# Kernel tuning notes

Hardware: AMD Instinct MI355X
Metric: run time of the kernel (lower is better)

## Reference

```python
import jax, jax.numpy as jnp
import numpy as np

ALPHA = 0.2      # leaky_alpha
GRAPH_ITR = 2    # graph_itr
ENC_LEN = 250    # output_begin_idx = encoder_sequence.shape[1]


def _char_embedding(ids, emb, conv_w, conv_b):
    # ids: [B,N,Wl] int -> char-CNN: embed, conv1d over word dim, relu, max-pool
    x = emb[ids]                                      # [B,N,Wl,E]
    B, N, Wl, E = x.shape
    x = x.reshape(B * N, Wl, E).transpose(0, 2, 1)    # [B*N, E, Wl]
    y = jax.lax.conv_general_dilated(x, conv_w, (1,), [(2, 2)],
                                     dimension_numbers=('NCH', 'OIH', 'NCH'))
    y = jax.nn.relu(y + conv_b[None, :, None])        # [B*N, F, Wl]
    return y.max(axis=2).reshape(B, N, -1)            # [B,N,F]


def _dynamic_graph(x, W0a, W0b, b0, W1, b1, Wout, bout):
    # Pairwise MLP on concat(x_i, x_j); first layer computed as split matmuls
    # so the [B,N,N,2d] concat is never materialized.
    hi = jnp.einsum('bnd,de->bne', x, W0a)            # [B,N,d]
    hj = jnp.einsum('bnd,de->bne', x, W0b)            # [B,N,d]
    h = jax.nn.relu(hi[:, :, None, :] + hj[:, None, :, :] + b0)   # [B,N,N,d]
    h = jax.nn.relu(jnp.einsum('bnme,ef->bnmf', h, W1) + b1)      # [B,N,N,d]
    return jax.nn.sigmoid(jnp.einsum('bnme,e->bnm', h, Wout[:, 0]) + bout[0])


def _gat(x, adj, W, a1, a2):
    # Multi-head GAT: per-head projection, additive attention, adjacency-masked softmax.
    Wh = jnp.einsum('bnd,hdk->bhnk', x, W)            # [B,H,N,hid]
    f1 = jnp.einsum('bhnk,hk->bhn', Wh, a1)
    f2 = jnp.einsum('bhnk,hk->bhn', Wh, a2)
    e = jax.nn.leaky_relu(f1[:, :, :, None] + f2[:, :, None, :], ALPHA)  # [B,H,N,N]
    e = jnp.where(adj[:, None, :, :] > 0, e, -9e15)
    attn = jax.nn.softmax(e, axis=-1)
    h = jax.nn.elu(jnp.einsum('bhnm,bhmk->bhnk', attn, Wh))
    B, H, N, K = h.shape
    return h.transpose(0, 2, 1, 3).reshape(B, N, H * K)  # concat heads -> [B,N,d]


def setup_inputs() -> dict:
    key = jax.random.key(0)
    ks = jax.random.split(key, 20)
    B, Le, Ld, Wl = 2, 250, 150, 16
    Vin, E, F, K = 128, 64, 128, 5
    H, hid, Vout = 8, 32, 5000
    d = H * hid  # 256
    s = lambda k, sh: jax.random.normal(k, sh, dtype=jnp.float32) * 0.05
    return {
        'encoder_sequence': jax.random.randint(ks[0], (B, Le, Wl), 0, Vin),
        'initial_decoder_sequence': jax.random.randint(ks[1], (B, Ld, Wl), 0, Vin),
        'fixed_graph': jax.random.randint(ks[2], (B, Le + Ld, Le + Ld), 0, 2),
        'char_emb': s(ks[3], (Vin, E)),
        'conv_w': s(ks[4], (F, E, K)),
        'conv_b': jnp.zeros((F,), jnp.float32),
        'hst_W': s(ks[5], (F, d)),
        'hst_b': jnp.zeros((d,), jnp.float32),
        'dg_W0a': s(ks[6], (d, d)),
        'dg_W0b': s(ks[7], (d, d)),
        'dg_b0': jnp.zeros((d,), jnp.float32),
        'dg_W1': s(ks[8], (d, d)),
        'dg_b1': jnp.zeros((d,), jnp.float32),
        'dg_Wout': s(ks[9], (d, 1)),
        'dg_bout': jnp.zeros((1,), jnp.float32),
        'att_W': s(ks[10], (H, d, hid)),
        'att_a1': s(ks[11], (H, hid)),
        'att_a2': s(ks[12], (H, hid)),
        'out_W': s(ks[13], (d, Vout)),
        'out_b': jnp.zeros((Vout,), jnp.float32),
    }


def reference(encoder_sequence, initial_decoder_sequence, fixed_graph,
              char_emb, conv_w, conv_b, hst_W, hst_b,
              dg_W0a, dg_W0b, dg_b0, dg_W1, dg_b1, dg_Wout, dg_bout,
              att_W, att_a1, att_a2, out_W, out_b):
    ids = jnp.concatenate([encoder_sequence, initial_decoder_sequence], axis=1)  # [B,N,Wl]
    x = _char_embedding(ids, char_emb, conv_w, conv_b)    # [B,N,F]
    x = x @ hst_W + hst_b                                 # [B,N,d]
    fixed = fixed_graph.astype(jnp.float32)
    for _ in range(GRAPH_ITR):
        dyn = _dynamic_graph(x, dg_W0a, dg_W0b, dg_b0, dg_W1, dg_b1, dg_Wout, dg_bout)
        adj = jnp.clip(dyn + fixed, 0.0, 1.0)             # combine dynamic + fixed graph
        x = _gat(x, adj, att_W, att_a1, att_a2)
    return x[:, ENC_LEN:, :] @ out_W + out_b              # [B, dec_len, Vout]
```

## Files before the change

### kernel.cpp

```cpp
#include <hip/hip_runtime.h>
#include <hip/hip_bf16.h>
#include <math.h>


__device__ __forceinline__ float bf2f_raw(unsigned int u) {
    union { unsigned int i; float f; } cv; cv.i = u << 16; return cv.f;
}
__device__ __forceinline__ unsigned short f2bf(float f) {
    __hip_bfloat16 h = __float2bfloat16(f);
    return *reinterpret_cast<unsigned short*>(&h);
}

__global__ __launch_bounds__(256) void k_prep(const float* emb, const float* convw,
                                              float* T, const float* W,
                                              unsigned short* Wb) {
    int bid = blockIdx.x, t = threadIdx.x;
    if (bid < 128) {
        int v = bid;
        __shared__ float er[64];
        if (t < 64) er[t] = emb[v * 64 + t];
        __syncthreads();
        if (t < 128) {
            float acc[5] = {0.f, 0.f, 0.f, 0.f, 0.f};
            const float* w = convw + t * 320;
            for (int e = 0; e < 64; ++e) {
                float xe = er[e];
#pragma unroll
                for (int k = 0; k < 5; ++k) acc[k] += xe * w[e * 5 + k];
            }
#pragma unroll
            for (int k = 0; k < 5; ++k) T[(k * 128 + v) * 128 + t] = acc[k];
        }
    } else {
        int i0 = (bid - 128) * 512 + t * 2;
        if (i0 < 256 * 5000) {
            float2 w2 = *reinterpret_cast<const float2*>(W + i0);
            unsigned int u = ((unsigned int)f2bf(w2.y) << 16) | f2bf(w2.x);
            *reinterpret_cast<unsigned int*>(Wb + i0) = u;
        }
    }
}

__global__ __launch_bounds__(256) void k_convhst(const int* enc, const int* dec,
                                                 const float* convb, const float* T,
                                                 const float* hstW, const float* hstb,
                                                 float* x) {
    int w = blockIdx.x, t = threadIdx.x;
    int b = w / 400, n = w % 400;
    __shared__ int ids[16];
    __shared__ float xcl[128];
    if (t < 16) {
        ids[t] = (n < 250) ? enc[(b * 250 + n) * 16 + t]
                           : dec[(b * 150 + (n - 250)) * 16 + t];
    }
    __syncthreads();
    if (t < 128) {
        float best = -1e30f;
        for (int p = 0; p < 16; ++p) {
            float s = 0.f;
#pragma unroll
            for (int k = 0; k < 5; ++k) {
                int q = p + k - 2;
                if (q >= 0 && q < 16) s += T[(k * 128 + ids[q]) * 128 + t];
            }
            best = fmaxf(best, s);
        }
        xcl[t] = fmaxf(best + convb[t], 0.f);
    }
    __syncthreads();
    float acc = hstb[t];
    for (int c = 0; c < 128; ++c) acc += xcl[c] * hstW[c * 256 + t];
    x[w * 256 + t] = acc;
}

__global__ __launch_bounds__(256) void k_wh(const float* x, const float* attW,
                                            const float* a1g, const float* a2g,
                                            float* Wh, float* f1, float* f2) {
    int blk = blockIdx.x, t = threadIdx.x;
    int w0 = blk * 2;
    int h = t >> 5, k = t & 31;
    __shared__ float xr[2][256];
    for (int i = t; i < 512; i += 256) xr[i >> 8][i & 255] = x[w0 * 256 + i];
    __syncthreads();
    float acc0 = 0.f, acc1 = 0.f;
    const float* Wp = attW + h * 8192 + k;
#pragma unroll 8
    for (int d = 0; d < 256; ++d) {
        float wv = Wp[d * 32];
        acc0 += xr[0][d] * wv;
        acc1 += xr[1][d] * wv;
    }
    float a1v = a1g[t], a2v = a2g[t];
    int b = w0 / 400;
    int bh = b * 8 + h;
    float accs[2] = {acc0, acc1};
#pragma unroll
    for (int rw = 0; rw < 2; ++rw) {
        int n = (w0 + rw) % 400;
        Wh[(bh * 400 + n) * 32 + k] = accs[rw];
        float v1 = accs[rw] * a1v, v2 = accs[rw] * a2v;
#pragma unroll
        for (int mm = 16; mm >= 1; mm >>= 1) {
            v1 += __shfl_xor(v1, mm, 64);
            v2 += __shfl_xor(v2, mm, 64);
        }
        if (k == 0) { f1[bh * 400 + n] = v1; f2[bh * 400 + n] = v2; }
    }
}

#define WST 36
__global__ __launch_bounds__(256) void k_attn(const float* Wh, const float* f1g,
                                              const float* f2g, float* xout) {
    int tile = blockIdx.x, bh = blockIdx.y;
    int b = bh >> 3, h = bh & 7;
    int t = threadIdx.x;
    int n0 = tile * 16;
    __shared__ float Whl[400 * WST];
    __shared__ float f2l[400];
    __shared__ float4 plT[400];
    __shared__ float f1l[16];
    __shared__ float red[4][8][4][4];
    __shared__ float sred[2][4][4];
    __shared__ float wmax[4];

    const float4* Whg4 = (const float4*)(Wh + bh * 12800);
    for (int i = t; i < 3200; i += 256) {
        float4 v = Whg4[i];
        int m = i >> 3, k4 = i & 7;
        *(float4*)&Whl[m * WST + k4 * 4] = v;
    }
    float fm = -1e30f;
    for (int m = t; m < 400; m += 256) {
        float v = f2g[bh * 400 + m];
        f2l[m] = v;
        fm = fmaxf(fm, v);
    }
    if (t < 16) f1l[t] = f1g[bh * 400 + n0 + t];
#pragma unroll
    for (int mm = 32; mm >= 1; mm >>= 1) fm = fmaxf(fm, __shfl_xor(fm, mm, 64));
    if ((t & 63) == 0) wmax[t >> 6] = fm;
    __syncthreads();
    float fmax2 = fmaxf(fmaxf(wmax[0], wmax[1]), fmaxf(wmax[2], wmax[3]));

    int g = t & 7, kq = (t >> 3) & 7, wv = t >> 6;
    int gm = g + 8 * wv;
    for (int it = 0; it < 4; ++it) {
        float f1a = f1l[it * 4 + 0], f1b = f1l[it * 4 + 1];
        float f1c = f1l[it * 4 + 2], f1d = f1l[it * 4 + 3];
        float rm0 = f1a + fmax2; rm0 = rm0 > 0.f ? rm0 : 0.2f * rm0;
        float rm1 = f1b + fmax2; rm1 = rm1 > 0.f ? rm1 : 0.2f * rm1;
        float rm2 = f1c + fmax2; rm2 = rm2 > 0.f ? rm2 : 0.2f * rm2;
        float rm3 = f1d + fmax2; rm3 = rm3 > 0.f ? rm3 : 0.2f * rm3;
        float ps0 = 0.f, ps1 = 0.f, ps2 = 0.f, ps3 = 0.f;
        for (int m = t; m < 400; m += 256) {
            float f2v = f2l[m];
            float e0 = f1a + f2v; e0 = e0 > 0.f ? e0 : 0.2f * e0;
            float e1 = f1b + f2v; e1 = e1 > 0.f ? e1 : 0.2f * e1;
            float e2 = f1c + f2v; e2 = e2 > 0.f ? e2 : 0.2f * e2;
            float e3 = f1d + f2v; e3 = e3 > 0.f ? e3 : 0.2f * e3;
            float4 pv;
            pv.x = __expf(e0 - rm0); ps0 += pv.x;
            pv.y = __expf(e1 - rm1); ps1 += pv.y;
            pv.z = __expf(e2 - rm2); ps2 += pv.z;
            pv.w = __expf(e3 - rm3); ps3 += pv.w;
            plT[m] = pv;
        }
        {
            float v0 = ps0, v1 = ps1, v2 = ps2, v3 = ps3;
#pragma unroll
            for (int mm = 32; mm >= 1; mm >>= 1) {
                v0 += __shfl_xor(v0, mm, 64);
                v1 += __shfl_xor(v1, mm, 64);
                v2 += __shfl_xor(v2, mm, 64);
                v3 += __shfl_xor(v3, mm, 64);
            }
            if ((t & 63) == 0) {
                int wq = t >> 6;
                sred[it & 1][0][wq] = v0; sred[it & 1][1][wq] = v1;
                sred[it & 1][2][wq] = v2; sred[it & 1][3][wq] = v3;
            }
        }
        __syncthreads();
        float a[4][4];
#pragma unroll
        for (int rr = 0; rr < 4; ++rr)
#pragma unroll
            for (int c = 0; c < 4; ++c) a[rr][c] = 0.f;
        for (int m = gm; m < 400; m += 32) {
            float4 w4 = *(const float4*)&Whl[m * WST + kq * 4];
            float4 p4 = plT[m];
            a[0][0] += p4.x * w4.x; a[0][1] += p4.x * w4.y; a[0][2] += p4.x * w4.z; a[0][3] += p4.x * w4.w;
            a[1][0] += p4.y * w4.x; a[1][1] += p4.y * w4.y; a[1][2] += p4.y * w4.z; a[1][3] += p4.y * w4.w;
            a[2][0] += p4.z * w4.x; a[2][1] += p4.z * w4.y; a[2][2] += p4.z * w4.z; a[2][3] += p4.z * w4.w;
            a[3][0] += p4.w * w4.x; a[3][1] += p4.w * w4.y; a[3][2] += p4.w * w4.z; a[3][3] += p4.w * w4.w;
        }
#pragma unroll
        for (int rr = 0; rr < 4; ++rr)
#pragma unroll
            for (int c = 0; c < 4; ++c) {
                float v = a[rr][c];
                v += __shfl_xor(v, 1, 64);
                v += __shfl_xor(v, 2, 64);
                v += __shfl_xor(v, 4, 64);
                a[rr][c] = v;
            }
        if (g == 0) {
#pragma unroll
            for (int rr = 0; rr < 4; ++rr)
#pragma unroll
                for (int c = 0; c < 4; ++c) red[wv][kq][rr][c] = a[rr][c];
        }
        __syncthreads();
        if (t < 128) {
            int rw3 = t >> 5, kk = t & 31;
            int q3 = kk >> 2, c3 = kk & 3;
            float s = sred[it & 1][rw3][0] + sred[it & 1][rw3][1]
                    + sred[it & 1][rw3][2] + sred[it & 1][rw3][3];
            float o = (red[0][q3][rw3][c3] + red[1][q3][rw3][c3]
                     + red[2][q3][rw3][c3] + red[3][q3][rw3][c3]) / s;
            o = o > 0.f ? o : (__expf(o) - 1.f);
            int n = n0 + it * 4 + rw3;
            xout[(b * 400 + n) * 256 + h * 32 + kk] = o;
        }
    }
}

__global__ __launch_bounds__(256) void k_out(const float* x, const unsigned short* Wb,
                                             const float* bias, float* out) {
    int vt = blockIdx.x, rg = blockIdx.y, t = threadIdx.x;
    __shared__ float xr[6][256];
    int r0 = rg * 6;
    int b = r0 / 150, n0 = 250 + (r0 % 150);
    for (int i = t; i < 1536; i += 256) {
        int rr = i >> 8, dd = i & 255;
        xr[rr][dd] = x[(b * 400 + n0 + rr) * 256 + dd];
    }
    __syncthreads();
    int v = vt * 512 + t * 2;
    if (v >= 5000) return;
    float acc[6][2];
#pragma unroll
    for (int rr = 0; rr < 6; ++rr) { acc[rr][0] = 0.f; acc[rr][1] = 0.f; }
    const unsigned short* Wp = Wb + v;
#pragma unroll 8
    for (int dd = 0; dd < 256; ++dd) {
        unsigned int wu = *reinterpret_cast<const unsigned int*>(Wp + dd * 5000);
        float w0 = bf2f_raw(wu & 0xFFFFu);
        float w1 = bf2f_raw(wu >> 16);
#pragma unroll
        for (int rr = 0; rr < 6; ++rr) {
            float xv = xr[rr][dd];
            acc[rr][0] += xv * w0;
            acc[rr][1] += xv * w1;
        }
    }
    float b0 = bias[v], b1 = bias[v + 1];
#pragma unroll
    for (int rr = 0; rr < 6; ++rr) {
        out[(r0 + rr) * 5000 + v]     = acc[rr][0] + b0;
        out[(r0 + rr) * 5000 + v + 1] = acc[rr][1] + b1;
    }
}

extern "C" void kernel_launch(void* const* d_in, const int* in_sizes, int n_in,
                              void* d_out, int out_size, void* d_ws, size_t ws_size,
                              hipStream_t stream) {
    const int*   enc   = (const int*)d_in[0];
    const int*   dec   = (const int*)d_in[1];
    const float* emb   = (const float*)d_in[3];
    const float* convw = (const float*)d_in[4];
    const float* convb = (const float*)d_in[5];
    const float* hstW  = (const float*)d_in[6];
    const float* hstb  = (const float*)d_in[7];
    const float* attW  = (const float*)d_in[15];
    const float* a1    = (const float*)d_in[16];
    const float* a2    = (const float*)d_in[17];
    const float* outW  = (const float*)d_in[18];
    const float* outb  = (const float*)d_in[19];
    float* out = (float*)d_out;

    char* ws = (char*)d_ws;
    float* T   = (float*)ws; ws += 5 * 128 * 128 * 4;
    float* xA  = (float*)ws; ws += 800 * 256 * 4;
    float* xB  = (float*)ws; ws += 800 * 256 * 4;
    float* Wh  = (float*)ws; ws += 16 * 400 * 32 * 4;
    float* f1  = (float*)ws; ws += 16 * 400 * 4;
    float* f2  = (float*)ws; ws += 16 * 400 * 4;
    unsigned short* Wb = (unsigned short*)ws; ws += 256 * 5000 * 2;

    k_prep<<<2628, 256, 0, stream>>>(emb, convw, T, outW, Wb);
    k_convhst<<<800, 256, 0, stream>>>(enc, dec, convb, T, hstW, hstb, xA);

    float* xin = xA;
    float* xo  = xB;
    for (int it = 0; it < 2; ++it) {
        k_wh<<<400, 256, 0, stream>>>(xin, attW, a1, a2, Wh, f1, f2);
        k_attn<<<dim3(25, 16), 256, 0, stream>>>(Wh, f1, f2, xo);
        float* tmp = xin; xin = xo; xo = tmp;
    }
    k_out<<<dim3(10, 50), 256, 0, stream>>>(xin, Wb, outb, out);
}
```

Before: 103.5 us.

## Stream Wh from global in attention and process two words per conv block

The attention kernel no longer stages the full per-head Wh matrix (400x36 floats) in shared memory. It reads Wh directly from global/L2 with float4 loads and halves the row tile to 8 rows, doubling the grid to 800 blocks. This cuts LDS use and the staging cost per block, which should raise occupancy, but each block now issues repeated global reads of Wh. Separately, the conv+projection kernel handles two words per block, so each hstW load is reused twice and all 256 threads do useful conv work.

```diff
diff --git a/kernel.cpp b/kernel.cpp
--- a/kernel.cpp
+++ b/kernel.cpp
@@ -45,32 +45,40 @@
                                                  const float* convb, const float* T,
                                                  const float* hstW, const float* hstb,
                                                  float* x) {
-    int w = blockIdx.x, t = threadIdx.x;
-    int b = w / 400, n = w % 400;
-    __shared__ int ids[16];
-    __shared__ float xcl[128];
-    if (t < 16) {
-        ids[t] = (n < 250) ? enc[(b * 250 + n) * 16 + t]
-                           : dec[(b * 150 + (n - 250)) * 16 + t];
-    }
-    __syncthreads();
-    if (t < 128) {
+    int w0 = blockIdx.x * 2, t = threadIdx.x;
+    __shared__ int ids[2][16];
+    __shared__ float xcl[2][128];
+    if (t < 32) {
+        int r = t >> 4, c = t & 15;
+        int w = w0 + r;
+        int b = w / 400, n = w % 400;
+        ids[r][c] = (n < 250) ? enc[(b * 250 + n) * 16 + c]
+                              : dec[(b * 150 + (n - 250)) * 16 + c];
+    }
+    __syncthreads();
+    {
+        int r = t >> 7, f = t & 127;
         float best = -1e30f;
         for (int p = 0; p < 16; ++p) {
             float s = 0.f;
 #pragma unroll
             for (int k = 0; k < 5; ++k) {
                 int q = p + k - 2;
-                if (q >= 0 && q < 16) s += T[(k * 128 + ids[q]) * 128 + t];
+                if (q >= 0 && q < 16) s += T[(k * 128 + ids[r][q]) * 128 + f];
             }
             best = fmaxf(best, s);
         }
-        xcl[t] = fmaxf(best + convb[t], 0.f);
-    }
-    __syncthreads();
-    float acc = hstb[t];
-    for (int c = 0; c < 128; ++c) acc += xcl[c] * hstW[c * 256 + t];
-    x[w * 256 + t] = acc;
+        xcl[r][f] = fmaxf(best + convb[f], 0.f);
+    }
+    __syncthreads();
+    float acc0 = hstb[t], acc1 = acc0;
+    for (int c = 0; c < 128; ++c) {
+        float wv = hstW[c * 256 + t];
+        acc0 += xcl[0][c] * wv;
+        acc1 += xcl[1][c] * wv;
+    }
+    x[w0 * 256 + t] = acc0;
+    x[(w0 + 1) * 256 + t] = acc1;
 }
 
 __global__ __launch_bounds__(256) void k_wh(const float* x, const float* attW,
@@ -108,34 +116,26 @@
     }
 }
 
-#define WST 36
 __global__ __launch_bounds__(256) void k_attn(const float* Wh, const float* f1g,
                                               const float* f2g, float* xout) {
     int tile = blockIdx.x, bh = blockIdx.y;
     int b = bh >> 3, h = bh & 7;
     int t = threadIdx.x;
-    int n0 = tile * 16;
-    __shared__ float Whl[400 * WST];
+    int n0 = tile * 8;
     __shared__ float f2l[400];
     __shared__ float4 plT[400];
-    __shared__ float f1l[16];
+    __shared__ float f1l[8];
     __shared__ float red[4][8][4][4];
     __shared__ float sred[2][4][4];
     __shared__ float wmax[4];
 
-    const float4* Whg4 = (const float4*)(Wh + bh * 12800);
-    for (int i = t; i < 3200; i += 256) {
-        float4 v = Whg4[i];
-        int m = i >> 3, k4 = i & 7;
-        *(float4*)&Whl[m * WST + k4 * 4] = v;
-    }
     float fm = -1e30f;
     for (int m = t; m < 400; m += 256) {
         float v = f2g[bh * 400 + m];
         f2l[m] = v;
         fm = fmaxf(fm, v);
     }
-    if (t < 16) f1l[t] = f1g[bh * 400 + n0 + t];
+    if (t < 8) f1l[t] = f1g[bh * 400 + n0 + t];
 #pragma unroll
     for (int mm = 32; mm >= 1; mm >>= 1) fm = fmaxf(fm, __shfl_xor(fm, mm, 64));
     if ((t & 63) == 0) wmax[t >> 6] = fm;
@@ -144,7 +144,8 @@
 
     int g = t & 7, kq = (t >> 3) & 7, wv = t >> 6;
     int gm = g + 8 * wv;
-    for (int it = 0; it < 4; ++it) {
+    const float4* WhG = (const float4*)(Wh + bh * 12800);
+    for (int it = 0; it < 2; ++it) {
         float f1a = f1l[it * 4 + 0], f1b = f1l[it * 4 + 1];
         float f1c = f1l[it * 4 + 2], f1d = f1l[it * 4 + 3];
         float rm0 = f1a + fmax2; rm0 = rm0 > 0.f ? rm0 : 0.2f * rm0;
@@ -186,8 +187,9 @@
         for (int rr = 0; rr < 4; ++rr)
 #pragma unroll
             for (int c = 0; c < 4; ++c) a[rr][c] = 0.f;
+#pragma unroll 4
         for (int m = gm; m < 400; m += 32) {
-            float4 w4 = *(const float4*)&Whl[m * WST + kq * 4];
+            float4 w4 = WhG[m * 8 + kq];
             float4 p4 = plT[m];
             a[0][0] += p4.x * w4.x; a[0][1] += p4.x * w4.y; a[0][2] += p4.x * w4.z; a[0][3] += p4.x * w4.w;
             a[1][0] += p4.y * w4.x; a[1][1] += p4.y * w4.y; a[1][2] += p4.y * w4.z; a[1][3] += p4.y * w4.w;
@@ -289,13 +291,13 @@
     unsigned short* Wb = (unsigned short*)ws; ws += 256 * 5000 * 2;
 
     k_prep<<<2628, 256, 0, stream>>>(emb, convw, T, outW, Wb);
-    k_convhst<<<800, 256, 0, stream>>>(enc, dec, convb, T, hstW, hstb, xA);
+    k_convhst<<<400, 256, 0, stream>>>(enc, dec, convb, T, hstW, hstb, xA);
 
     float* xin = xA;
     float* xo  = xB;
     for (int it = 0; it < 2; ++it) {
         k_wh<<<400, 256, 0, stream>>>(xin, attW, a1, a2, Wh, f1, f2);
-        k_attn<<<dim3(25, 16), 256, 0, stream>>>(Wh, f1, f2, xo);
+        k_attn<<<dim3(50, 16), 256, 0, stream>>>(Wh, f1, f2, xo);
         float* tmp = xin; xin = xo; xo = tmp;
     }
     k_out<<<dim3(10, 50), 256, 0, stream>>>(xin, Wb, outb, out);
```

Result: faster. 101.3 us (-2.1%).
